# Kernel optimization log

Hardware: AMD Instinct MI355X
Metric: run time of the kernel (lower is better)

## Reference

```python
import jax, jax.numpy as jnp
import numpy as np
from jax import lax

GAMMA = 0.99
LAM = 0.95


def setup_inputs() -> dict:
    key = jax.random.key(0)
    k1, k2, k3 = jax.random.split(key, 3)
    B, S = 4096, 4096
    rewards = jax.random.normal(k1, (B, S), dtype=jnp.float32)
    values = jax.random.normal(k2, (B, S), dtype=jnp.float32)
    next_values = jax.random.normal(k3, (B,), dtype=jnp.float32)
    return {"rewards": rewards, "values": values, "next_values": next_values}


def reference(rewards, values, next_values):
    # delta_t = r_t + gamma * V(s_{t+1}) - V(s_t); bootstrap with next_values at t = S-1
    next_v_full = jnp.concatenate([values[:, 1:], next_values[:, None]], axis=1)  # [B,S]
    deltas = rewards + GAMMA * next_v_full - values  # [B,S]

    # Reverse-time recurrence: A_t = delta_t + gamma*lam * A_{t+1}
    def step(adv, delta_t):
        adv = delta_t + (GAMMA * LAM) * adv
        return adv, adv

    deltas_rev = jnp.swapaxes(deltas, 0, 1)[::-1]  # [S,B], time-reversed
    init = jnp.zeros(rewards.shape[0], dtype=rewards.dtype)
    _, advs_rev = lax.scan(step, init, deltas_rev)  # [S,B]
    advantages = jnp.swapaxes(advs_rev[::-1], 0, 1)  # [B,S]

    returns = advantages + values
    # original detaches both outputs
    return (lax.stop_gradient(advantages), lax.stop_gradient(returns))
```

## Files before the change

kernel.cpp:

```cpp
#include <hip/hip_runtime.h>


#define GAMMA 0.99f
#define LAM   0.95f

constexpr int S_LEN = 4096;
constexpr int TPB   = 256;
constexpr int CHUNK = S_LEN / TPB;

__global__ __launch_bounds__(TPB) void gae_kernel(const float* __restrict__ rewards,
                                                  const float* __restrict__ values,
                                                  const float* __restrict__ next_values,
                                                  float* __restrict__ out, int B) {
    __shared__ float vals[S_LEN];
    __shared__ float rews[S_LEN];
    __shared__ float waveT[4];

    const int b   = blockIdx.x;
    const int tid = threadIdx.x;
    const float c = GAMMA * LAM;

    const float* vrow = values  + (size_t)b * S_LEN;
    const float* rrow = rewards + (size_t)b * S_LEN;

#pragma unroll
    for (int j = 0; j < CHUNK / 4; ++j) {
        int idx = j * TPB + tid;
        ((float4*)vals)[idx] = ((const float4*)vrow)[idx];
        ((float4*)rews)[idx] = ((const float4*)rrow)[idx];
    }
    const float nv = next_values[b];
    __syncthreads();

    const int base = tid * CHUNK;
    float a[CHUNK];
    float acc = 0.f;
#pragma unroll
    for (int li = CHUNK - 1; li >= 0; --li) {
        int i = base + li;
        float vnext = (i == S_LEN - 1) ? nv : vals[i + 1];
        float delta = rews[i] + GAMMA * vnext - vals[i];
        acc = delta + c * acc;
        a[li] = acc;
    }
    float v = acc;

    float q = 1.f;
#pragma unroll
    for (int k = 0; k < CHUNK; ++k) q *= c;

    const int lane = tid & 63;
    const int wave = tid >> 6;
    float x = v;
    float qs[6];
    float qd = q;
#pragma unroll
    for (int dlog = 0; dlog < 6; ++dlog) {
        int d = 1 << dlog;
        qs[dlog] = qd;
        float other = __shfl_down(x, d);
        if (lane + d < 64) x += qd * other;
        qd *= qd;
    }
    const float Q = qd;

    if (lane == 0) waveT[wave] = x;
    __syncthreads();
    float t0 = waveT[0], t1 = waveT[1], t2 = waveT[2], t3 = waveT[3];
    (void)t0;
    float F3 = t3;
    float F2 = t2 + Q * F3;
    float F1 = t1 + Q * F2;
    float carry_wave = (wave == 3) ? 0.f : (wave == 2 ? F3 : (wave == 1 ? F2 : F1));

    float Wnext = __shfl_down(x, 1);
    int e = 63 - lane;
    float qp = 1.f;
#pragma unroll
    for (int k = 0; k < 6; ++k) qp *= ((e >> k) & 1) ? qs[k] : 1.f;
    float C = (lane == 63) ? carry_wave : fmaf(qp, carry_wave, Wnext);

    float p = c;
#pragma unroll
    for (int li = CHUNK - 1; li >= 0; --li) {
        a[li] = fmaf(p, C, a[li]);
        p *= c;
    }

    __syncthreads();
#pragma unroll
    for (int li = 0; li < CHUNK; ++li) rews[base + li] = a[li];
    __syncthreads();

    float* adv_row = out + (size_t)b * S_LEN;
    float* ret_row = out + (size_t)B * S_LEN + (size_t)b * S_LEN;
#pragma unroll
    for (int j = 0; j < CHUNK / 4; ++j) {
        int idx = j * TPB + tid;
        float4 av = ((float4*)rews)[idx];
        float4 vv = ((float4*)vals)[idx];
        float4 rv = make_float4(av.x + vv.x, av.y + vv.y, av.z + vv.z, av.w + vv.w);
        ((float4*)adv_row)[idx] = av;
        ((float4*)ret_row)[idx] = rv;
    }
}

extern "C" void kernel_launch(void* const* d_in, const int* in_sizes, int n_in,
                              void* d_out, int out_size, void* d_ws, size_t ws_size,
                              hipStream_t stream) {
    const float* rewards     = (const float*)d_in[0];
    const float* values      = (const float*)d_in[1];
    const float* next_values = (const float*)d_in[2];
    float* out = (float*)d_out;
    const int B = in_sizes[2];
    gae_kernel<<<B, TPB, 0, stream>>>(rewards, values, next_values, out, B);
}
```

Measured before the change: 44.93 us.

## Load row chunks directly into registers, bypassing shared-memory staging

New measurement: 59.29 us. 32.0% more time.

```diff
diff --git a/kernel.cpp b/kernel.cpp
--- a/kernel.cpp
+++ b/kernel.cpp
@@ -12,38 +12,46 @@
                                                   const float* __restrict__ values,
                                                   const float* __restrict__ next_values,
                                                   float* __restrict__ out, int B) {
-    __shared__ float vals[S_LEN];
-    __shared__ float rews[S_LEN];
     __shared__ float waveT[4];
 
     const int b   = blockIdx.x;
     const int tid = threadIdx.x;
     const float c = GAMMA * LAM;
 
-    const float* vrow = values  + (size_t)b * S_LEN;
-    const float* rrow = rewards + (size_t)b * S_LEN;
+    const size_t rowoff = (size_t)b * S_LEN + (size_t)tid * CHUNK;
+    const float* vrow = values  + rowoff;
+    const float* rrow = rewards + rowoff;
 
+    float4 v4[4], r4[4];
 #pragma unroll
-    for (int j = 0; j < CHUNK / 4; ++j) {
-        int idx = j * TPB + tid;
-        ((float4*)vals)[idx] = ((const float4*)vrow)[idx];
-        ((float4*)rews)[idx] = ((const float4*)rrow)[idx];
+    for (int j = 0; j < 4; ++j) v4[j] = ((const float4*)vrow)[j];
+#pragma unroll
+    for (int j = 0; j < 4; ++j) r4[j] = ((const float4*)rrow)[j];
+    const float vtail = (tid == TPB - 1) ? next_values[b] : vrow[CHUNK];
+
+    float v[CHUNK + 1];
+#pragma unroll
+    for (int j = 0; j < 4; ++j) {
+        v[4 * j + 0] = v4[j].x; v[4 * j + 1] = v4[j].y;
+        v[4 * j + 2] = v4[j].z; v[4 * j + 3] = v4[j].w;
     }
-    const float nv = next_values[b];
-    __syncthreads();
+    v[CHUNK] = vtail;
+    float r[CHUNK];
+#pragma unroll
+    for (int j = 0; j < 4; ++j) {
+        r[4 * j + 0] = r4[j].x; r[4 * j + 1] = r4[j].y;
+        r[4 * j + 2] = r4[j].z; r[4 * j + 3] = r4[j].w;
+    }
 
-    const int base = tid * CHUNK;
     float a[CHUNK];
     float acc = 0.f;
 #pragma unroll
     for (int li = CHUNK - 1; li >= 0; --li) {
-        int i = base + li;
-        float vnext = (i == S_LEN - 1) ? nv : vals[i + 1];
-        float delta = rews[i] + GAMMA * vnext - vals[i];
-        acc = delta + c * acc;
+        float delta = fmaf(GAMMA, v[li + 1], r[li]) - v[li];
+        acc = fmaf(c, acc, delta);
         a[li] = acc;
     }
-    float v = acc;
+    float x = acc;
 
     float q = 1.f;
 #pragma unroll
@@ -51,7 +59,6 @@
 
     const int lane = tid & 63;
     const int wave = tid >> 6;
-    float x = v;
     float qs[6];
     float qd = q;
 #pragma unroll
@@ -59,18 +66,17 @@
         int d = 1 << dlog;
         qs[dlog] = qd;
         float other = __shfl_down(x, d);
-        if (lane + d < 64) x += qd * other;
+        if (lane + d < 64) x = fmaf(qd, other, x);
         qd *= qd;
     }
     const float Q = qd;
 
     if (lane == 0) waveT[wave] = x;
     __syncthreads();
-    float t0 = waveT[0], t1 = waveT[1], t2 = waveT[2], t3 = waveT[3];
-    (void)t0;
+    float t1 = waveT[1], t2 = waveT[2], t3 = waveT[3];
     float F3 = t3;
-    float F2 = t2 + Q * F3;
-    float F1 = t1 + Q * F2;
+    float F2 = fmaf(Q, F3, t2);
+    float F1 = fmaf(Q, F2, t1);
     float carry_wave = (wave == 3) ? 0.f : (wave == 2 ? F3 : (wave == 1 ? F2 : F1));
 
     float Wnext = __shfl_down(x, 1);
@@ -87,21 +93,15 @@
         p *= c;
     }
 
-    __syncthreads();
+    float* adv_row = out + rowoff;
+    float* ret_row = out + (size_t)B * S_LEN + rowoff;
 #pragma unroll
-    for (int li = 0; li < CHUNK; ++li) rews[base + li] = a[li];
-    __syncthreads();
-
-    float* adv_row = out + (size_t)b * S_LEN;
-    float* ret_row = out + (size_t)B * S_LEN + (size_t)b * S_LEN;
-#pragma unroll
-    for (int j = 0; j < CHUNK / 4; ++j) {
-        int idx = j * TPB + tid;
-        float4 av = ((float4*)rews)[idx];
-        float4 vv = ((float4*)vals)[idx];
-        float4 rv = make_float4(av.x + vv.x, av.y + vv.y, av.z + vv.z, av.w + vv.w);
-        ((float4*)adv_row)[idx] = av;
-        ((float4*)ret_row)[idx] = rv;
+    for (int j = 0; j < 4; ++j) {
+        float4 av = make_float4(a[4 * j + 0], a[4 * j + 1], a[4 * j + 2], a[4 * j + 3]);
+        ((float4*)adv_row)[j] = av;
+        float4 rv = make_float4(av.x + v[4 * j + 0], av.y + v[4 * j + 1],
+                                av.z + v[4 * j + 2], av.w + v[4 * j + 3]);
+        ((float4*)ret_row)[j] = rv;
     }
 }
 
```

## Scan GAE in registers with 4-element-per-thread segments, removing LDS staging

Applied to the files above, without the earlier changes.

Result: no change. 45.34 us (+0.9%).

```diff
diff --git a/kernel.cpp b/kernel.cpp
--- a/kernel.cpp
+++ b/kernel.cpp
@@ -6,102 +6,114 @@
 
 constexpr int S_LEN = 4096;
 constexpr int TPB   = 256;
-constexpr int CHUNK = S_LEN / TPB;
+constexpr int NSEG  = 4;
 
 __global__ __launch_bounds__(TPB) void gae_kernel(const float* __restrict__ rewards,
                                                   const float* __restrict__ values,
                                                   const float* __restrict__ next_values,
                                                   float* __restrict__ out, int B) {
-    __shared__ float vals[S_LEN];
-    __shared__ float rews[S_LEN];
-    __shared__ float waveT[4];
+    __shared__ float Tlds[16];
 
-    const int b   = blockIdx.x;
-    const int tid = threadIdx.x;
-    const float c = GAMMA * LAM;
+    const int b    = blockIdx.x;
+    const int tid  = threadIdx.x;
+    const int lane = tid & 63;
+    const int w    = tid >> 6;
+    const float c  = GAMMA * LAM;
+    const float q4 = c * c * c * c;
 
     const float* vrow = values  + (size_t)b * S_LEN;
     const float* rrow = rewards + (size_t)b * S_LEN;
+    const float  nv   = next_values[b];
+
+    float4 v4[NSEG], r4[NSEG];
+    float  vn[NSEG];
+#pragma unroll
+    for (int s = 0; s < NSEG; ++s) {
+        const int g0 = s * 1024 + 4 * tid;
+        v4[s] = *(const float4*)(vrow + g0);
+        r4[s] = *(const float4*)(rrow + g0);
+    }
+#pragma unroll
+    for (int s = 0; s < NSEG; ++s) {
+        const int g4 = s * 1024 + 4 * tid + 4;
+        if (s == NSEG - 1 && tid == TPB - 1) vn[s] = nv;
+        else                                 vn[s] = vrow[g4];
+    }
+
+    float a0[NSEG], a1[NSEG], a2[NSEG], a3[NSEG];
+    float Wn[NSEG];
+    float Tk = 0.f;
+    float qs[6];
+    {
+        float qd = q4;
+#pragma unroll
+        for (int k = 0; k < 6; ++k) { qs[k] = qd; qd *= qd; }
+    }
+    const float Q256 = qs[5] * qs[5];
 
 #pragma unroll
-    for (int j = 0; j < CHUNK / 4; ++j) {
-        int idx = j * TPB + tid;
-        ((float4*)vals)[idx] = ((const float4*)vrow)[idx];
-        ((float4*)rews)[idx] = ((const float4*)rrow)[idx];
-    }
-    const float nv = next_values[b];
-    __syncthreads();
+    for (int s = 0; s < NSEG; ++s) {
+        float d3 = fmaf(GAMMA, vn[s],   r4[s].w) - v4[s].w;
+        float d2 = fmaf(GAMMA, v4[s].w, r4[s].z) - v4[s].z;
+        float d1 = fmaf(GAMMA, v4[s].z, r4[s].y) - v4[s].y;
+        float d0 = fmaf(GAMMA, v4[s].y, r4[s].x) - v4[s].x;
+        float t3 = d3;
+        float t2 = fmaf(c, t3, d2);
+        float t1 = fmaf(c, t2, d1);
+        float t0 = fmaf(c, t1, d0);
+        a3[s] = t3; a2[s] = t2; a1[s] = t1; a0[s] = t0;
 
-    const int base = tid * CHUNK;
-    float a[CHUNK];
-    float acc = 0.f;
+        float x = t0;
 #pragma unroll
-    for (int li = CHUNK - 1; li >= 0; --li) {
-        int i = base + li;
-        float vnext = (i == S_LEN - 1) ? nv : vals[i + 1];
-        float delta = rews[i] + GAMMA * vnext - vals[i];
-        acc = delta + c * acc;
-        a[li] = acc;
-    }
-    float v = acc;
-
-    float q = 1.f;
-#pragma unroll
-    for (int k = 0; k < CHUNK; ++k) q *= c;
-
-    const int lane = tid & 63;
-    const int wave = tid >> 6;
-    float x = v;
-    float qs[6];
-    float qd = q;
-#pragma unroll
-    for (int dlog = 0; dlog < 6; ++dlog) {
-        int d = 1 << dlog;
-        qs[dlog] = qd;
-        float other = __shfl_down(x, d);
-        if (lane + d < 64) x += qd * other;
-        qd *= qd;
-    }
-    const float Q = qd;
-
-    if (lane == 0) waveT[wave] = x;
-    __syncthreads();
-    float t0 = waveT[0], t1 = waveT[1], t2 = waveT[2], t3 = waveT[3];
-    (void)t0;
-    float F3 = t3;
-    float F2 = t2 + Q * F3;
-    float F1 = t1 + Q * F2;
-    float carry_wave = (wave == 3) ? 0.f : (wave == 2 ? F3 : (wave == 1 ? F2 : F1));
-
-    float Wnext = __shfl_down(x, 1);
-    int e = 63 - lane;
-    float qp = 1.f;
-#pragma unroll
-    for (int k = 0; k < 6; ++k) qp *= ((e >> k) & 1) ? qs[k] : 1.f;
-    float C = (lane == 63) ? carry_wave : fmaf(qp, carry_wave, Wnext);
-
-    float p = c;
-#pragma unroll
-    for (int li = CHUNK - 1; li >= 0; --li) {
-        a[li] = fmaf(p, C, a[li]);
-        p *= c;
+        for (int dlog = 0; dlog < 6; ++dlog) {
+            int d = 1 << dlog;
+            float other = __shfl_down(x, d);
+            if (lane + d < 64) x = fmaf(qs[dlog], other, x);
+        }
+        Wn[s] = __shfl_down(x, 1);
+        float tb = __shfl(x, 0);
+        if (lane == s) Tk = tb;
     }
 
+    if (lane < NSEG) Tlds[lane * 4 + w] = Tk;
     __syncthreads();
+    float tv = (lane < 16) ? Tlds[lane] : 0.f;
+    {
+        float Qd = Q256;
 #pragma unroll
-    for (int li = 0; li < CHUNK; ++li) rews[base + li] = a[li];
-    __syncthreads();
+        for (int dlog = 0; dlog < 4; ++dlog) {
+            int d = 1 << dlog;
+            float other = __shfl_down(tv, d);
+            if (lane + d < 16) tv = fmaf(Qd, other, tv);
+            Qd *= Qd;
+        }
+    }
+
+    float qp = 1.f;
+    {
+        int e = 63 - lane;
+#pragma unroll
+        for (int k = 0; k < 6; ++k) if ((e >> k) & 1) qp *= qs[k];
+    }
 
     float* adv_row = out + (size_t)b * S_LEN;
     float* ret_row = out + (size_t)B * S_LEN + (size_t)b * S_LEN;
+    const float c2 = c * c, c3 = c2 * c;
 #pragma unroll
-    for (int j = 0; j < CHUNK / 4; ++j) {
-        int idx = j * TPB + tid;
-        float4 av = ((float4*)rews)[idx];
-        float4 vv = ((float4*)vals)[idx];
-        float4 rv = make_float4(av.x + vv.x, av.y + vv.y, av.z + vv.z, av.w + vv.w);
-        ((float4*)adv_row)[idx] = av;
-        ((float4*)ret_row)[idx] = rv;
+    for (int s = 0; s < NSEG; ++s) {
+        const int m = s * 4 + w;
+        float Cm = (m == 15) ? 0.f : __shfl(tv, m + 1);
+        float ct = (lane == 63) ? Cm : fmaf(qp, Cm, Wn[s]);
+        float o3 = fmaf(c,  ct, a3[s]);
+        float o2 = fmaf(c2, ct, a2[s]);
+        float o1 = fmaf(c3, ct, a1[s]);
+        float o0 = fmaf(q4, ct, a0[s]);
+        const int g0 = s * 1024 + 4 * tid;
+        float4 av = make_float4(o0, o1, o2, o3);
+        *(float4*)(adv_row + g0) = av;
+        float4 rv = make_float4(av.x + v4[s].x, av.y + v4[s].y,
+                                av.z + v4[s].z, av.w + v4[s].w);
+        *(float4*)(ret_row + g0) = rv;
     }
 }
 
```
